# Performance work log

Measured on AMD Instinct MI355X. Metric: run time of the kernel, lower is better.

The kernel has to match this reference:

```python
import jax, jax.numpy as jnp
import numpy as np

NA, NKPT, NC = 3, 17, 1
NO_DET = NC + 5              # 6
NO = NO_DET + 3 * NKPT       # 57
ANCHORS = np.array([[19,27,44,40,38,94],[96,68,86,152,180,137],[140,301,303,264,238,542]], dtype=np.float32).reshape(3, 3, 2)
STRIDES = np.array([8.0, 16.0, 32.0], dtype=np.float32)
CH = (256, 512, 1024)
HW = (80, 40, 20)
B = 16


def setup_inputs():
    key = jax.random.key(0)
    ks = jax.random.split(key, 18)
    d = {}
    ki = 0
    for i, (c, hw) in enumerate(zip(CH, HW)):
        d[f"f{i}"] = jax.random.normal(ks[ki], (B, c, hw, hw), jnp.float32); ki += 1
        d[f"ia{i}"] = jax.random.normal(ks[ki], (1, c, 1, 1), jnp.float32) * 0.02; ki += 1
        d[f"w{i}"] = jax.random.normal(ks[ki], (NA * NO_DET, c), jnp.float32) * (1.0 / np.sqrt(c)); ki += 1
        d[f"b{i}"] = jnp.zeros((NA * NO_DET,), jnp.float32)
        d[f"im{i}"] = 1.0 + jax.random.normal(ks[ki], (1, NA * NO_DET, 1, 1), jnp.float32) * 0.02; ki += 1
        d[f"wk{i}"] = jax.random.normal(ks[ki], (NA * 3 * NKPT, c), jnp.float32) * (1.0 / np.sqrt(c)); ki += 1
        d[f"bk{i}"] = jnp.zeros((NA * 3 * NKPT,), jnp.float32)
    return d


def _decode(feat, ia, w, b, im, wk, bk, anchors_l, stride):
    # ImplicitA -> 1x1 conv -> ImplicitM (det branch); plain 1x1 conv (kpt branch)
    det = jnp.einsum('bchw,oc->bohw', feat + ia, w) + b[None, :, None, None]
    det = det * im
    kpt = jnp.einsum('bchw,oc->bohw', feat, wk) + bk[None, :, None, None]
    x = jnp.concatenate([det, kpt], axis=1)          # (B, na*no, H, W)
    Bb, _, H, W = x.shape
    x = x.reshape(Bb, NA, NO, H, W).transpose(0, 1, 3, 4, 2)  # (B, na, H, W, no)
    yv, xv = jnp.meshgrid(jnp.arange(H), jnp.arange(W), indexing='ij')
    grid = jnp.stack([xv, yv], -1).astype(x.dtype)[None, None]  # (1,1,H,W,2)
    xd = jax.nn.sigmoid(x[..., :NO_DET])
    xy = (xd[..., 0:2] * 2.0 - 0.5 + grid) * stride
    wh = (xd[..., 2:4] * 2.0) ** 2 * anchors_l.reshape(1, NA, 1, 1, 2)
    kp = x[..., NO_DET:]                              # (B, na, H, W, 51)
    kx = (kp[..., 0::3] * 2.0 - 0.5 + grid[..., 0:1]) * stride
    ky = (kp[..., 1::3] * 2.0 - 0.5 + grid[..., 1:2]) * stride
    kc = jax.nn.sigmoid(kp[..., 2::3])
    kdec = jnp.stack([kx, ky, kc], -1).reshape(Bb, NA, H, W, 3 * NKPT)
    y = jnp.concatenate([xy, wh, xd[..., 4:], kdec], -1)  # (B, na, H, W, 57)
    return y.reshape(Bb, -1, NO)


def reference(f0, ia0, w0, b0, im0, wk0, bk0,
              f1, ia1, w1, b1, im1, wk1, bk1,
              f2, ia2, w2, b2, im2, wk2, bk2):
    anchors = jnp.asarray(ANCHORS)
    z0 = _decode(f0, ia0, w0, b0, im0, wk0, bk0, anchors[0], STRIDES[0])
    z1 = _decode(f1, ia1, w1, b1, im1, wk1, bk1, anchors[1], STRIDES[1])
    z2 = _decode(f2, ia2, w2, b2, im2, wk2, bk2, anchors[2], STRIDES[2])
    return jnp.concatenate([z0, z1, z2], axis=1)      # (B, 25200, 57)
```

## Files before the change

### kernel.cpp

```cpp
#include <hip/hip_runtime.h>
#include <hip/hip_bf16.h>

typedef __attribute__((ext_vector_type(8))) short short8;
typedef __attribute__((ext_vector_type(4))) float floatx4;

__device__ __forceinline__ float sigm(float x) { return 1.0f / (1.0f + __expf(-x)); }

__device__ __forceinline__ unsigned short f2bf(float v) {
  union { __hip_bfloat16 h; unsigned short u; } cv;
  cv.h = __float2bfloat16(v);
  return cv.u;
}

__device__ __forceinline__ void glds16(const void* g, void* l) {
  __builtin_amdgcn_global_load_lds((const __attribute__((address_space(1))) void*)g,
                                   (__attribute__((address_space(3))) void*)l, 16, 0, 0);
}

struct PrepArgs {
  const float *w, *b, *im, *ia, *wk, *bk;
  unsigned short* Wp;
  float* bias;
  int C;
};

__global__ void prep_kernel(PrepArgs A0, PrepArgs A1, PrepArgs A2) {
  PrepArgs A = (blockIdx.y == 0) ? A0 : (blockIdx.y == 1) ? A1 : A2;
  const int n = blockIdx.x;
  const int t = threadIdx.x;
  const int C = A.C;
  unsigned short* wrow = A.Wp + (size_t)n * C;
  if (n >= 171) {
    for (int k = t; k < C; k += 64) wrow[k] = 0;
    if (t == 0) A.bias[n] = 0.0f;
    return;
  }
  if (n < 18) {
    const float* src = A.w + (size_t)n * C;
    const float sc = A.im[n];
    float dot = 0.0f;
    for (int k = t; k < C; k += 64) {
      float v = src[k];
      dot += v * A.ia[k];
      wrow[k] = f2bf(v * sc);
    }
#pragma unroll
    for (int off = 32; off > 0; off >>= 1) dot += __shfl_down(dot, off);
    if (t == 0) A.bias[n] = sc * (A.b[n] + dot);
  } else {
    const float* src = A.wk + (size_t)(n - 18) * C;
    for (int k = t; k < C; k += 64) wrow[k] = f2bf(src[k]);
    if (t == 0) A.bias[n] = A.bk[n - 18];
  }
}

#define LDS_BYTES 34560

template <int SC, int C, int HW, int W>
__device__ __forceinline__ void gemm_decode(const float* __restrict__ feat,
                                            const unsigned short* __restrict__ Wp,
                                            const float* __restrict__ bias,
                                            float* __restrict__ out, int tile, char* smem) {
  constexpr float STRD = (SC == 0) ? 8.0f : (SC == 1) ? 16.0f : 32.0f;
  constexpr int ZOFF = (SC == 0) ? 0 : (SC == 1) ? 19200 : 24000;
  constexpr int I = C / 64;

  const int t = threadIdx.x;
  const int lane = t & 63;
  const int wv = t >> 6;
  const int l15 = lane & 15;
  const int quad = lane >> 4;

  unsigned short* Alds = (unsigned short*)smem;
  char* BB = smem + 9216;
  float* Elds = (float*)smem;

  const int mA = tile * 64 + lane;
  const int bA = mA / HW;
  const int pA = mA - bA * HW;
  const float* fbase = feat + ((size_t)bA * C + wv * 16) * (size_t)HW + pA;

  const int rsub = lane >> 3;
  const int csw = (lane & 7) ^ rsub;
  const char* WpB = (const char*)Wp;

  floatx4 acc[11];
#pragma unroll
  for (int nj = 0; nj < 11; ++nj) acc[nj] = (floatx4){0.f, 0.f, 0.f, 0.f};

  const unsigned short* aRd = Alds + (wv * 16 + l15) * 72 + quad * 8;
  const int c0 = quad ^ (l15 & 7);
  const char* bRd0 = BB + (size_t)l15 * 128 + c0 * 16;
  const char* bRd1 = BB + (size_t)l15 * 128 + (c0 ^ 4) * 16;

  float v[16];
  auto loadA = [&](int it) {
    const float* g = fbase + (size_t)it * 64 * HW;
#pragma unroll
    for (int kk = 0; kk < 16; ++kk) v[kk] = g[(size_t)kk * HW];
  };
  auto writeA = [&]() {
    short8 s0, s1;
#pragma unroll
    for (int j = 0; j < 8; ++j) {
      s0[j] = (short)f2bf(v[j]);
      s1[j] = (short)f2bf(v[j + 8]);
    }
    *(short8*)(Alds + lane * 72 + wv * 16) = s0;
    *(short8*)(Alds + lane * 72 + wv * 16 + 8) = s1;
  };

  loadA(0);
  for (int it = 0; it < I; ++it) {
    asm volatile("s_barrier" ::: "memory");
#pragma unroll
    for (int j = 0; j < 6; ++j) {
      const int rowb = wv * 48 + j * 8;
      const void* gsrc = WpB + ((size_t)(rowb + rsub) * C + (size_t)it * 64) * 2 + csw * 16;
      glds16(gsrc, BB + rowb * 128);
    }
    __builtin_amdgcn_sched_barrier(0);
    writeA();
    loadA((it + 1 < I) ? it + 1 : it);
    __builtin_amdgcn_sched_barrier(0);
    asm volatile("s_waitcnt vmcnt(16) lgkmcnt(0)\n\ts_barrier" ::: "memory");
    short8 af0 = *(const short8*)(aRd);
    short8 af1 = *(const short8*)(aRd + 32);
#pragma unroll
    for (int nj = 0; nj < 11; ++nj) {
      short8 b0 = *(const short8*)(bRd0 + (size_t)nj * 2048);
      short8 b1 = *(const short8*)(bRd1 + (size_t)nj * 2048);
      acc[nj] = __builtin_amdgcn_mfma_f32_16x16x32_bf16(af0, b0, acc[nj], 0, 0, 0);
      acc[nj] = __builtin_amdgcn_mfma_f32_16x16x32_bf16(af1, b1, acc[nj], 0, 0, 0);
    }
  }

  float bj[11];
#pragma unroll
  for (int nj = 0; nj < 11; ++nj) bj[nj] = bias[nj * 16 + l15];

#pragma unroll
  for (int c = 0; c < 2; ++c) {
    __syncthreads();
    if ((wv >> 1) == c) {
      const int rbase = (wv & 1) * 16 + quad * 4;
#pragma unroll
      for (int nj = 0; nj < 11; ++nj)
#pragma unroll
        for (int r = 0; r < 4; ++r)
          Elds[(rbase + r) * 180 + nj * 16 + l15] = acc[nj][r] + bj[nj];
    }
    __syncthreads();
    if (t < 192) {
      const int task = t >> 1, half = t & 1;
      const int row = task & 31, a = task >> 5;
      const int m = tile * 64 + c * 32 + row;
      const int bb = m / HW;
      const int p = m - bb * HW;
      const float fx = (float)(p % W);
      const float fy = (float)(p / W);
      float* L = Elds + row * 180 + a * 57;
      if (half == 0) {
        float aw, ah;
        if constexpr (SC == 0) {
          aw = (a == 0) ? 19.f : (a == 1) ? 44.f : 38.f;
          ah = (a == 0) ? 27.f : (a == 1) ? 40.f : 94.f;
        } else if constexpr (SC == 1) {
          aw = (a == 0) ? 96.f : (a == 1) ? 86.f : 180.f;
          ah = (a == 0) ? 68.f : (a == 1) ? 152.f : 137.f;
        } else {
          aw = (a == 0) ? 140.f : (a == 1) ? 303.f : 238.f;
          ah = (a == 0) ? 301.f : (a == 1) ? 264.f : 542.f;
        }
        float r0 = L[0], r1 = L[1], r2 = L[2], r3 = L[3], r4 = L[4], r5 = L[5];
        L[0] = (sigm(r0) * 2.f - 0.5f + fx) * STRD;
        L[1] = (sigm(r1) * 2.f - 0.5f + fy) * STRD;
        float tw = sigm(r2) * 2.f;
        L[2] = tw * tw * aw;
        float th = sigm(r3) * 2.f;
        L[3] = th * th * ah;
        L[4] = sigm(r4);
        L[5] = sigm(r5);
#pragma unroll
        for (int kp = 0; kp < 8; ++kp) {
          float kx = L[6 + 3 * kp], ky = L[7 + 3 * kp], kc = L[8 + 3 * kp];
          L[6 + 3 * kp] = (kx * 2.f - 0.5f + fx) * STRD;
          L[7 + 3 * kp] = (ky * 2.f - 0.5f + fy) * STRD;
          L[8 + 3 * kp] = sigm(kc);
        }
      } else {
#pragma unroll
        for (int kp = 8; kp < 17; ++kp) {
          float kx = L[6 + 3 * kp], ky = L[7 + 3 * kp], kc = L[8 + 3 * kp];
          L[6 + 3 * kp] = (kx * 2.f - 0.5f + fx) * STRD;
          L[7 + 3 * kp] = (ky * 2.f - 0.5f + fy) * STRD;
          L[8 + 3 * kp] = sigm(kc);
        }
      }
    }
    __syncthreads();
    for (int i = t; i < 96 * 57; i += 256) {
      int sr = i / 57;
      int j = i - sr * 57;
      int a = sr >> 5, row = sr & 31;
      int m = tile * 64 + c * 32 + row;
      int bb = m / HW;
      int p = m - bb * HW;
      out[((size_t)bb * 25200 + (size_t)(ZOFF + a * HW + p)) * 57 + j] =
          Elds[row * 180 + a * 57 + j];
    }
  }
}

__global__ __launch_bounds__(256, 4) void main_kernel(
    const float* __restrict__ f0, const float* __restrict__ f1, const float* __restrict__ f2,
    const unsigned short* __restrict__ Wp0, const unsigned short* __restrict__ Wp1,
    const unsigned short* __restrict__ Wp2, const float* __restrict__ b0,
    const float* __restrict__ b1, const float* __restrict__ b2, float* __restrict__ out) {
  __shared__ __align__(16) char smem[LDS_BYTES];
  const int bid = blockIdx.x;
  if (bid < 100)
    gemm_decode<2, 1024, 400, 20>(f2, Wp2, b2, out, bid, smem);
  else if (bid < 500)
    gemm_decode<1, 512, 1600, 40>(f1, Wp1, b1, out, bid - 100, smem);
  else
    gemm_decode<0, 256, 6400, 80>(f0, Wp0, b0, out, bid - 500, smem);
}

extern "C" void kernel_launch(void* const* d_in, const int* in_sizes, int n_in, void* d_out,
                              int out_size, void* d_ws, size_t ws_size, hipStream_t stream) {
  const float *f[3], *ia[3], *w[3], *b[3], *im[3], *wk[3], *bk[3];
  for (int s = 0; s < 3; ++s) {
    f[s] = (const float*)d_in[7 * s + 0];
    ia[s] = (const float*)d_in[7 * s + 1];
    w[s] = (const float*)d_in[7 * s + 2];
    b[s] = (const float*)d_in[7 * s + 3];
    im[s] = (const float*)d_in[7 * s + 4];
    wk[s] = (const float*)d_in[7 * s + 5];
    bk[s] = (const float*)d_in[7 * s + 6];
  }
  char* ws = (char*)d_ws;
  unsigned short* Wp0 = (unsigned short*)(ws + 0);
  unsigned short* Wp1 = (unsigned short*)(ws + 98304);
  unsigned short* Wp2 = (unsigned short*)(ws + 294912);
  float* bias0 = (float*)(ws + 688128);
  float* bias1 = (float*)(ws + 688896);
  float* bias2 = (float*)(ws + 689664);

  PrepArgs A0 = {w[0], b[0], im[0], ia[0], wk[0], bk[0], Wp0, bias0, 256};
  PrepArgs A1 = {w[1], b[1], im[1], ia[1], wk[1], bk[1], Wp1, bias1, 512};
  PrepArgs A2 = {w[2], b[2], im[2], ia[2], wk[2], bk[2], Wp2, bias2, 1024};
  prep_kernel<<<dim3(192, 3), 64, 0, stream>>>(A0, A1, A2);

  main_kernel<<<2100, 256, 0, stream>>>(f[0], f[1], f[2], Wp0, Wp1, Wp2, bias0, bias1, bias2,
                                        (float*)d_out);
}
```

Measured before the change: 297.0 us.

## Load GEMM operands directly into registers, removing LDS staging and barriers

The mainloop no longer stages A (features) and B (weights) through LDS with global_load_lds and barriers. Each lane now loads its own MFMA fragments straight from global memory: A is double-buffered in registers two iterations ahead, and B rows are read with a rolling three-deep register prefetch. The aim is to drop the LDS round trips and the per-iteration block syncs. The cost is redundant global/L2 traffic for the weights, since every wave reloads all of B, plus more register pressure. The LDS size and prep grid shrink to match.

```diff
diff --git a/kernel.cpp b/kernel.cpp
--- a/kernel.cpp
+++ b/kernel.cpp
@@ -10,11 +10,6 @@
   union { __hip_bfloat16 h; unsigned short u; } cv;
   cv.h = __float2bfloat16(v);
   return cv.u;
-}
-
-__device__ __forceinline__ void glds16(const void* g, void* l) {
-  __builtin_amdgcn_global_load_lds((const __attribute__((address_space(1))) void*)g,
-                                   (__attribute__((address_space(3))) void*)l, 16, 0, 0);
 }
 
 struct PrepArgs {
@@ -54,7 +49,7 @@
   }
 }
 
-#define LDS_BYTES 34560
+#define LDS_BYTES 23040
 
 template <int SC, int C, int HW, int W>
 __device__ __forceinline__ void gemm_decode(const float* __restrict__ feat,
@@ -71,68 +66,62 @@
   const int l15 = lane & 15;
   const int quad = lane >> 4;
 
-  unsigned short* Alds = (unsigned short*)smem;
-  char* BB = smem + 9216;
   float* Elds = (float*)smem;
 
-  const int mA = tile * 64 + lane;
-  const int bA = mA / HW;
-  const int pA = mA - bA * HW;
-  const float* fbase = feat + ((size_t)bA * C + wv * 16) * (size_t)HW + pA;
-
-  const int rsub = lane >> 3;
-  const int csw = (lane & 7) ^ rsub;
-  const char* WpB = (const char*)Wp;
+  const int mG = tile * 64 + wv * 16 + l15;
+  const int bA = mG / HW;
+  const int pA = mG - bA * HW;
+  const float* gA = feat + ((size_t)bA * C + quad * 8) * (size_t)HW + pA;
+
+  const unsigned short* bP = Wp + (size_t)l15 * C + quad * 8;
 
   floatx4 acc[11];
 #pragma unroll
   for (int nj = 0; nj < 11; ++nj) acc[nj] = (floatx4){0.f, 0.f, 0.f, 0.f};
 
-  const unsigned short* aRd = Alds + (wv * 16 + l15) * 72 + quad * 8;
-  const int c0 = quad ^ (l15 & 7);
-  const char* bRd0 = BB + (size_t)l15 * 128 + c0 * 16;
-  const char* bRd1 = BB + (size_t)l15 * 128 + (c0 ^ 4) * 16;
-
-  float v[16];
-  auto loadA = [&](int it) {
-    const float* g = fbase + (size_t)it * 64 * HW;
-#pragma unroll
-    for (int kk = 0; kk < 16; ++kk) v[kk] = g[(size_t)kk * HW];
+  auto loadA = [&](float (&dst)[16], int it) {
+    const float* g = gA + (size_t)it * 64 * HW;
+#pragma unroll
+    for (int j = 0; j < 8; ++j) {
+      dst[j] = g[(size_t)j * HW];
+      dst[j + 8] = g[(size_t)(j + 32) * HW];
+    }
   };
-  auto writeA = [&]() {
-    short8 s0, s1;
+
+  auto step = [&](float (&cur)[16], int it) {
+    const unsigned short* bI = bP + (size_t)it * 64;
+    short8 breg[3][2];
+#pragma unroll
+    for (int j = 0; j < 3; ++j) {
+      breg[j][0] = *(const short8*)(bI + (size_t)j * 16 * C);
+      breg[j][1] = *(const short8*)(bI + (size_t)j * 16 * C + 32);
+    }
+    short8 af0, af1;
 #pragma unroll
     for (int j = 0; j < 8; ++j) {
-      s0[j] = (short)f2bf(v[j]);
-      s1[j] = (short)f2bf(v[j + 8]);
-    }
-    *(short8*)(Alds + lane * 72 + wv * 16) = s0;
-    *(short8*)(Alds + lane * 72 + wv * 16 + 8) = s1;
-  };
-
-  loadA(0);
-  for (int it = 0; it < I; ++it) {
-    asm volatile("s_barrier" ::: "memory");
-#pragma unroll
-    for (int j = 0; j < 6; ++j) {
-      const int rowb = wv * 48 + j * 8;
-      const void* gsrc = WpB + ((size_t)(rowb + rsub) * C + (size_t)it * 64) * 2 + csw * 16;
-      glds16(gsrc, BB + rowb * 128);
-    }
-    __builtin_amdgcn_sched_barrier(0);
-    writeA();
-    loadA((it + 1 < I) ? it + 1 : it);
-    __builtin_amdgcn_sched_barrier(0);
-    asm volatile("s_waitcnt vmcnt(16) lgkmcnt(0)\n\ts_barrier" ::: "memory");
-    short8 af0 = *(const short8*)(aRd);
-    short8 af1 = *(const short8*)(aRd + 32);
+      af0[j] = (short)f2bf(cur[j]);
+      af1[j] = (short)f2bf(cur[j + 8]);
+    }
+    if (it + 2 < I) loadA(cur, it + 2);
 #pragma unroll
     for (int nj = 0; nj < 11; ++nj) {
-      short8 b0 = *(const short8*)(bRd0 + (size_t)nj * 2048);
-      short8 b1 = *(const short8*)(bRd1 + (size_t)nj * 2048);
+      short8 b0 = breg[nj % 3][0];
+      short8 b1 = breg[nj % 3][1];
+      if (nj + 3 < 11) {
+        breg[nj % 3][0] = *(const short8*)(bI + (size_t)(nj + 3) * 16 * C);
+        breg[nj % 3][1] = *(const short8*)(bI + (size_t)(nj + 3) * 16 * C + 32);
+      }
       acc[nj] = __builtin_amdgcn_mfma_f32_16x16x32_bf16(af0, b0, acc[nj], 0, 0, 0);
       acc[nj] = __builtin_amdgcn_mfma_f32_16x16x32_bf16(af1, b1, acc[nj], 0, 0, 0);
     }
+  };
+
+  float va[16], vb[16];
+  loadA(va, 0);
+  loadA(vb, 1);
+  for (int it = 0; it < I; it += 2) {
+    step(va, it);
+    step(vb, it + 1);
   }
 
   float bj[11];
@@ -250,7 +239,7 @@
   PrepArgs A0 = {w[0], b[0], im[0], ia[0], wk[0], bk[0], Wp0, bias0, 256};
   PrepArgs A1 = {w[1], b[1], im[1], ia[1], wk[1], bk[1], Wp1, bias1, 512};
   PrepArgs A2 = {w[2], b[2], im[2], ia[2], wk[2], bk[2], Wp2, bias2, 1024};
-  prep_kernel<<<dim3(192, 3), 64, 0, stream>>>(A0, A1, A2);
+  prep_kernel<<<dim3(176, 3), 64, 0, stream>>>(A0, A1, A2);
 
   main_kernel<<<2100, 256, 0, stream>>>(f[0], f[1], f[2], Wp0, Wp1, Wp2, bias0, bias1, bias2,
                                         (float*)d_out);
```

Measured after the change: 392.3 us. 1.32x slower.
